# Kernel tuning notes

Hardware: AMD Instinct MI355X
Metric: run time of the kernel (lower is better)

Reference implementation:

```python
import jax, jax.numpy as jnp
import numpy as np

E, D, H = 16, 2048, 2048

def setup_inputs() -> dict:
    key = jax.random.key(0)
    ks = jax.random.split(key, 8)
    s = 0.02
    return {
        "x":  jax.random.normal(ks[0], (D,), dtype=jnp.float32),
        "Wg": jax.random.normal(ks[1], (E, D), dtype=jnp.float32) * s,
        "bg": jnp.zeros((E,), dtype=jnp.float32),
        "W1": jax.random.normal(ks[2], (E, H, D), dtype=jnp.float32) * s,
        "b1": jnp.zeros((E, H), dtype=jnp.float32),
        "W2": jax.random.normal(ks[3], (E, H, H), dtype=jnp.float32) * s,
        "b2": jnp.zeros((E, H), dtype=jnp.float32),
        "train": 0,
    }

def reference(x, Wg, bg, W1, b1, W2, b2, train):
    # Gating: softmax over experts (eval path: no noise since train=0)
    logits = Wg @ x + bg                       # [E]
    gate = jax.nn.softmax(logits)              # [E]
    vals, idx = jax.lax.top_k(gate, 2)         # [2], [2]
    tkg = vals / (vals.sum() + 1e-6)           # normalized top-2 gates [2]
    # Only the two selected experts contribute (others are zeroed in the
    # original); compute just those two experts.
    h = jnp.tanh(jnp.einsum('khd,d->kh', W1[idx], x) + b1[idx])   # [2,H]
    eo = jnp.einsum('koh,kh->ko', W2[idx], h) + b2[idx]           # [2,H]
    out = jnp.einsum('k,kh->h', tkg, eo)                          # [H]
    return out
```

## Files before the change

kernel.cpp:

```cpp
#include <hip/hip_runtime.h>
#include <cmath>

#define E_EXPERTS 16
#define D_DIM 2048
#define H_DIM 2048

__global__ __launch_bounds__(256) void moe_gate_h(
    const float* __restrict__ x,  const float* __restrict__ Wg,
    const float* __restrict__ bg, const float* __restrict__ W1,
    const float* __restrict__ b1, float* __restrict__ ws) {
    float* tkg = ws;
    int*   idx = ((int*)ws) + 2;
    float* h   = ws + 16;

    const int tid  = threadIdx.x;
    const int wave = tid >> 6;
    const int lane = tid & 63;
    const int blk  = blockIdx.x;

    __shared__ float slog[E_EXPERTS];

    const float4* xv = (const float4*)x;
    float4 xx[8];
#pragma unroll
    for (int i = 0; i < 8; ++i) xx[i] = xv[lane + i * 64];

#pragma unroll
    for (int q = 0; q < 4; ++q) {
        const int e = wave * 4 + q;
        const float4* wrow = (const float4*)(Wg + (size_t)e * D_DIM);
        float acc = 0.f;
#pragma unroll
        for (int i = 0; i < 8; ++i) {
            float4 w = wrow[lane + i * 64];
            acc += w.x * xx[i].x + w.y * xx[i].y + w.z * xx[i].z + w.w * xx[i].w;
        }
#pragma unroll
        for (int off = 32; off; off >>= 1) acc += __shfl_down(acc, off, 64);
        if (lane == 0) slog[e] = acc + bg[e];
    }
    __syncthreads();

    float m = -1e30f;
#pragma unroll
    for (int e = 0; e < E_EXPERTS; ++e) m = fmaxf(m, slog[e]);
    float p[E_EXPERTS];
    float s = 0.f;
#pragma unroll
    for (int e = 0; e < E_EXPERTS; ++e) { p[e] = __expf(slog[e] - m); s += p[e]; }
    int i0 = 0; float v0 = p[0];
#pragma unroll
    for (int e = 1; e < E_EXPERTS; ++e) if (p[e] > v0) { v0 = p[e]; i0 = e; }
    int i1 = -1; float v1 = -1.f;
#pragma unroll
    for (int e = 0; e < E_EXPERTS; ++e) {
        if (e == i0) continue;
        if (p[e] > v1) { v1 = p[e]; i1 = e; }
    }
    float g0 = v0 / s, g1 = v1 / s;
    float denom = g0 + g1 + 1e-6f;

    if (blk == 0 && tid == 0) {
        tkg[0] = g0 / denom;
        tkg[1] = g1 / denom;
        idx[0] = i0;
        idx[1] = i1;
    }

    const int gw = blk * 4 + wave;
    const int k  = gw >> 11;
    const int r  = gw & (H_DIM - 1);
    const int e  = (k == 0) ? i0 : i1;

    const float4* wrow = (const float4*)(W1 + ((size_t)e * H_DIM + r) * D_DIM);
    float acc = 0.f;
#pragma unroll
    for (int i = 0; i < 8; ++i) {
        float4 w = wrow[lane + i * 64];
        acc += w.x * xx[i].x + w.y * xx[i].y + w.z * xx[i].z + w.w * xx[i].w;
    }
#pragma unroll
    for (int off = 32; off; off >>= 1) acc += __shfl_down(acc, off, 64);
    if (lane == 0) h[k * H_DIM + r] = tanhf(acc + b1[(size_t)e * H_DIM + r]);
}

__global__ __launch_bounds__(256) void moe_out(
    const float* __restrict__ W2, const float* __restrict__ b2,
    const float* __restrict__ ws, float* __restrict__ out) {
    const float* tkg = ws;
    const int*   idx = ((const int*)ws) + 2;
    const float* h   = ws + 16;

    const int tid  = threadIdx.x;
    const int wave = tid >> 6;
    const int lane = tid & 63;
    const int blk  = blockIdx.x;

    const int o = blk * 2 + (wave & 1);
    const int k = wave >> 1;
    const int e = idx[k];

    __shared__ float sred[4];

    const float4* wrow = (const float4*)(W2 + ((size_t)e * H_DIM + o) * H_DIM);
    const float4* hv   = (const float4*)(h + k * H_DIM);
    float acc = 0.f;
#pragma unroll
    for (int i = 0; i < 8; ++i) {
        float4 w  = wrow[lane + i * 64];
        float4 hh = hv[lane + i * 64];
        acc += w.x * hh.x + w.y * hh.y + w.z * hh.z + w.w * hh.w;
    }
#pragma unroll
    for (int off = 32; off; off >>= 1) acc += __shfl_down(acc, off, 64);
    if (lane == 0) sred[wave] = acc;
    __syncthreads();

    if (tid < 2) {
        const int oo = blk * 2 + tid;
        const int e0 = idx[0], e1 = idx[1];
        float eo0 = sred[tid]     + b2[(size_t)e0 * H_DIM + oo];
        float eo1 = sred[2 + tid] + b2[(size_t)e1 * H_DIM + oo];
        out[oo] = tkg[0] * eo0 + tkg[1] * eo1;
    }
}

extern "C" void kernel_launch(void* const* d_in, const int* in_sizes, int n_in,
                              void* d_out, int out_size, void* d_ws, size_t ws_size,
                              hipStream_t stream) {
    const float* x  = (const float*)d_in[0];
    const float* Wg = (const float*)d_in[1];
    const float* bg = (const float*)d_in[2];
    const float* W1 = (const float*)d_in[3];
    const float* b1 = (const float*)d_in[4];
    const float* W2 = (const float*)d_in[5];
    const float* b2 = (const float*)d_in[6];
    float* out  = (float*)d_out;
    float* ws_f = (float*)d_ws;

    moe_gate_h<<<1024, 256, 0, stream>>>(x, Wg, bg, W1, b1, ws_f);
    moe_out<<<1024, 256, 0, stream>>>(W2, b2, ws_f, out);
}
```

Before: 24.33 us.

## Compute gate logits once in a separate kernel instead of per block

Before, each of the 1024 blocks in the first kernel recomputed all 16 gate logits by reading the full Wg matrix. The gate dot products now run in a dedicated 16-block kernel that writes the logits to workspace. The hidden-layer and output kernels each recompute softmax and top-2 from those 16 logits. This removes redundant Wg traffic and compute at the cost of an extra kernel launch and a serial dependency between launches.

```diff
diff --git a/kernel.cpp b/kernel.cpp
--- a/kernel.cpp
+++ b/kernel.cpp
@@ -5,53 +5,49 @@
 #define D_DIM 2048
 #define H_DIM 2048
 
-__global__ __launch_bounds__(256) void moe_gate_h(
-    const float* __restrict__ x,  const float* __restrict__ Wg,
-    const float* __restrict__ bg, const float* __restrict__ W1,
-    const float* __restrict__ b1, float* __restrict__ ws) {
-    float* tkg = ws;
-    int*   idx = ((int*)ws) + 2;
-    float* h   = ws + 16;
 
+__global__ __launch_bounds__(256) void gate_logits(
+    const float* __restrict__ Wg, const float* __restrict__ bg,
+    const float* __restrict__ x, float* __restrict__ logits) {
     const int tid  = threadIdx.x;
     const int wave = tid >> 6;
     const int lane = tid & 63;
-    const int blk  = blockIdx.x;
+    const int e    = blockIdx.x;
 
-    __shared__ float slog[E_EXPERTS];
+    __shared__ float sred[4];
 
-    const float4* xv = (const float4*)x;
-    float4 xx[8];
+    const float4* wrow = (const float4*)(Wg + (size_t)e * D_DIM);
+    const float4* xv   = (const float4*)x;
+    float acc = 0.f;
 #pragma unroll
-    for (int i = 0; i < 8; ++i) xx[i] = xv[lane + i * 64];
+    for (int i = 0; i < 2; ++i) {
+        float4 w  = wrow[tid + i * 256];
+        float4 xx = xv[tid + i * 256];
+        acc += w.x * xx.x + w.y * xx.y + w.z * xx.z + w.w * xx.w;
+    }
+#pragma unroll
+    for (int off = 32; off; off >>= 1) acc += __shfl_down(acc, off, 64);
+    if (lane == 0) sred[wave] = acc;
+    __syncthreads();
+    if (tid == 0) logits[e] = sred[0] + sred[1] + sred[2] + sred[3] + bg[e];
+}
 
+__device__ __forceinline__ void top2_from_logits(
+    const float* __restrict__ logits, int& i0, int& i1, float& tk0, float& tk1) {
+    float l[E_EXPERTS];
 #pragma unroll
-    for (int q = 0; q < 4; ++q) {
-        const int e = wave * 4 + q;
-        const float4* wrow = (const float4*)(Wg + (size_t)e * D_DIM);
-        float acc = 0.f;
-#pragma unroll
-        for (int i = 0; i < 8; ++i) {
-            float4 w = wrow[lane + i * 64];
-            acc += w.x * xx[i].x + w.y * xx[i].y + w.z * xx[i].z + w.w * xx[i].w;
-        }
-#pragma unroll
-        for (int off = 32; off; off >>= 1) acc += __shfl_down(acc, off, 64);
-        if (lane == 0) slog[e] = acc + bg[e];
-    }
-    __syncthreads();
-
+    for (int e = 0; e < E_EXPERTS; ++e) l[e] = logits[e];
     float m = -1e30f;
 #pragma unroll
-    for (int e = 0; e < E_EXPERTS; ++e) m = fmaxf(m, slog[e]);
+    for (int e = 0; e < E_EXPERTS; ++e) m = fmaxf(m, l[e]);
     float p[E_EXPERTS];
     float s = 0.f;
 #pragma unroll
-    for (int e = 0; e < E_EXPERTS; ++e) { p[e] = __expf(slog[e] - m); s += p[e]; }
-    int i0 = 0; float v0 = p[0];
+    for (int e = 0; e < E_EXPERTS; ++e) { p[e] = __expf(l[e] - m); s += p[e]; }
+    i0 = 0; float v0 = p[0];
 #pragma unroll
     for (int e = 1; e < E_EXPERTS; ++e) if (p[e] > v0) { v0 = p[e]; i0 = e; }
-    int i1 = -1; float v1 = -1.f;
+    i1 = -1; float v1 = -1.f;
 #pragma unroll
     for (int e = 0; e < E_EXPERTS; ++e) {
         if (e == i0) continue;
@@ -59,15 +55,29 @@
     }
     float g0 = v0 / s, g1 = v1 / s;
     float denom = g0 + g1 + 1e-6f;
+    tk0 = g0 / denom;
+    tk1 = g1 / denom;
+}
 
-    if (blk == 0 && tid == 0) {
-        tkg[0] = g0 / denom;
-        tkg[1] = g1 / denom;
-        idx[0] = i0;
-        idx[1] = i1;
-    }
+__global__ __launch_bounds__(256) void moe_h(
+    const float* __restrict__ x,  const float* __restrict__ W1,
+    const float* __restrict__ b1, float* __restrict__ ws) {
+    const float* logits = ws;
+    float* h = ws + 16;
 
-    const int gw = blk * 4 + wave;
+    const int tid  = threadIdx.x;
+    const int wave = tid >> 6;
+    const int lane = tid & 63;
+
+    const float4* xv = (const float4*)x;
+    float4 xx[8];
+#pragma unroll
+    for (int i = 0; i < 8; ++i) xx[i] = xv[lane + i * 64];
+
+    int i0, i1; float tk0, tk1;
+    top2_from_logits(logits, i0, i1, tk0, tk1);
+
+    const int gw = blockIdx.x * 4 + wave;
     const int k  = gw >> 11;
     const int r  = gw & (H_DIM - 1);
     const int e  = (k == 0) ? i0 : i1;
@@ -87,18 +97,19 @@
 __global__ __launch_bounds__(256) void moe_out(
     const float* __restrict__ W2, const float* __restrict__ b2,
     const float* __restrict__ ws, float* __restrict__ out) {
-    const float* tkg = ws;
-    const int*   idx = ((const int*)ws) + 2;
-    const float* h   = ws + 16;
+    const float* logits = ws;
+    const float* h = ws + 16;
 
     const int tid  = threadIdx.x;
     const int wave = tid >> 6;
     const int lane = tid & 63;
-    const int blk  = blockIdx.x;
 
-    const int o = blk * 2 + (wave & 1);
+    int i0, i1; float tk0, tk1;
+    top2_from_logits(logits, i0, i1, tk0, tk1);
+
+    const int o = blockIdx.x * 2 + (wave & 1);
     const int k = wave >> 1;
-    const int e = idx[k];
+    const int e = (k == 0) ? i0 : i1;
 
     __shared__ float sred[4];
 
@@ -117,11 +128,10 @@
     __syncthreads();
 
     if (tid < 2) {
-        const int oo = blk * 2 + tid;
-        const int e0 = idx[0], e1 = idx[1];
-        float eo0 = sred[tid]     + b2[(size_t)e0 * H_DIM + oo];
-        float eo1 = sred[2 + tid] + b2[(size_t)e1 * H_DIM + oo];
-        out[oo] = tkg[0] * eo0 + tkg[1] * eo1;
+        const int oo = blockIdx.x * 2 + tid;
+        float eo0 = sred[tid]     + b2[(size_t)i0 * H_DIM + oo];
+        float eo1 = sred[2 + tid] + b2[(size_t)i1 * H_DIM + oo];
+        out[oo] = tk0 * eo0 + tk1 * eo1;
     }
 }
 
@@ -138,6 +148,7 @@
     float* out  = (float*)d_out;
     float* ws_f = (float*)d_ws;
 
-    moe_gate_h<<<1024, 256, 0, stream>>>(x, Wg, bg, W1, b1, ws_f);
+    gate_logits<<<16, 256, 0, stream>>>(Wg, bg, x, ws_f);
+    moe_h<<<1024, 256, 0, stream>>>(x, W1, b1, ws_f);
     moe_out<<<1024, 256, 0, stream>>>(W2, b2, ws_f, out);
 }
```

Result: no change. 24.73 us (+1.6%).
